# Optimization experiments

Hardware: AMD Instinct MI355X
Metric: run time of the kernel (lower is better)

## Reference

```python
import jax, jax.numpy as jnp
import numpy as np

B, S, D, VOCAB = 1024, 200, 128, 100000
MIN_LEN = 10


def setup_inputs() -> dict:
    key = jax.random.key(0)
    k1, k2, k3 = jax.random.split(key, 3)
    # variable per-row lengths; nonzero tokens contiguous at sequence start (right-padded)
    lengths = jax.random.randint(k1, (B,), MIN_LEN, S + 1)
    vals = jax.random.randint(k2, (B, S), 1, VOCAB)
    pos = jnp.arange(S)
    seqs = jnp.where(pos[None, :] < lengths[:, None], vals, 0)
    seq_embeddings = jax.random.normal(k3, (B, S, D), dtype=jnp.float32)
    return {"seqs": seqs, "seq_embeddings": seq_embeddings}


def _fft_prob(seqs):
    # Per-row: binary indicator of (token == last real token) over the L real
    # tokens, length-L DFT magnitude, zero last bin, normalize, roll by 1,
    # zero-pad to S. Variable-length FFT is written as an explicit DFT so the
    # whole batch is one dense einsum (same math as torch.fft.fft on length L).
    b, s = seqs.shape
    pos = jnp.arange(s)
    L = jnp.sum(seqs != 0, axis=1)                       # [B] real lengths
    last = seqs[jnp.arange(b), L - 1]                    # last real POI per row
    valid = pos[None, :] < L[:, None]                    # [B,S]
    binary = ((seqs == last[:, None]) & valid).astype(jnp.float32)  # [B,S]
    # DFT_k = sum_{n<L} binary_n * exp(-2*pi*i*k*n/L); binary is 0 for n>=L
    kn = (pos[:, None] * pos[None, :]).astype(jnp.float32)           # [S,S]
    theta = (-2.0 * jnp.pi) * kn[None, :, :] / L[:, None, None].astype(jnp.float32)  # [B,S,S]
    re = jnp.einsum('bkn,bn->bk', jnp.cos(theta), binary)
    im = jnp.einsum('bkn,bn->bk', jnp.sin(theta), binary)
    mag = jnp.sqrt(re * re + im * im)                    # [B,S] |FFT|
    # fft_prob[-1] = 0 (bin L-1) and bins k>=L are padding -> keep k < L-1
    keep = pos[None, :] < (L - 1)[:, None]
    mag = jnp.where(keep, mag, 0.0)
    prob = mag / jnp.sum(mag, axis=1, keepdims=True)
    # torch.roll(shifts=1) over the length-L vector: rolled[0]=prob[L-1]=0,
    # rolled[k]=prob[k-1]; since prob[k]=0 for k>=L-1 this equals a global
    # right-shift-by-one with zero fill, then implicit zero pad to S.
    rolled = jnp.pad(prob[:, :-1], ((0, 0), (1, 0)))
    return rolled                                         # [B,S]


def reference(seqs, seq_embeddings):
    prob = _fft_prob(seqs)                                # [B,S]
    return jnp.einsum('bs,bsd->bd', prob, seq_embeddings)  # [B,D]
```

## Files before the change

### kernel.cpp

```cpp
#include <hip/hip_runtime.h>
#include <math.h>

#define BATCH 1024
#define SEQ   200
#define DIM   128

__global__ __launch_bounds__(256) void dft_layer_kernel(
    const int* __restrict__ seqs,
    const float* __restrict__ emb,
    float* __restrict__ out)
{
    const int b   = blockIdx.x;
    const int tid = threadIdx.x;

    __shared__ int   s_seq[SEQ];
    __shared__ float s_mag[SEQ];
    __shared__ int   s_match[SEQ];
    __shared__ int   s_cnt[2];
    __shared__ float s_sum;
    __shared__ float s_part[8][DIM];

    if (tid < 2)  s_cnt[tid] = 0;
    if (tid == 0) s_sum = 0.0f;
    if (tid < SEQ) s_seq[tid] = seqs[b * SEQ + tid];
    __syncthreads();

    bool nz = (tid < SEQ) && (s_seq[tid] != 0);
    unsigned long long bal = __ballot(nz);
    if ((tid & 63) == 0) atomicAdd(&s_cnt[0], __popcll(bal));
    __syncthreads();

    const int L    = s_cnt[0];
    const int last = s_seq[L - 1];

    if (tid < L && s_seq[tid] == last) {
        int idx = atomicAdd(&s_cnt[1], 1);
        s_match[idx] = tid;
    }
    __syncthreads();
    const int   M  = s_cnt[1];
    const float Lf = (float)L;

    float mag = 0.0f;
    if (tid < SEQ) {
        if (tid < L - 1) {
            float re = 0.0f, im = 0.0f;
            const float kf = (float)tid;
            for (int m = 0; m < M; ++m) {
                float kn    = kf * (float)s_match[m];
                float theta = (-6.2831855f * kn) / Lf;
                float sv, cv;
                sincosf(theta, &sv, &cv);
                re += cv;
                im += sv;
            }
            mag = sqrtf(re * re + im * im);
        }
        s_mag[tid] = mag;
    }
    float v = mag;
    #pragma unroll
    for (int o = 32; o > 0; o >>= 1) v += __shfl_down(v, o, 64);
    if ((tid & 63) == 0) atomicAdd(&s_sum, v);
    __syncthreads();
    const float invSum = 1.0f / s_sum;

    const int c4 = tid & 31;
    const int g  = tid >> 5;
    const float4* ebase = (const float4*)(emb + (size_t)b * SEQ * DIM);
    float4 acc = make_float4(0.f, 0.f, 0.f, 0.f);
    for (int s = 1 + g; s < L; s += 8) {
        float  w = s_mag[s - 1];
        float4 e = ebase[s * 32 + c4];
        acc.x += w * e.x; acc.y += w * e.y; acc.z += w * e.z; acc.w += w * e.w;
    }
    {
        float* p = &s_part[g][c4 << 2];
        p[0] = acc.x; p[1] = acc.y; p[2] = acc.z; p[3] = acc.w;
    }
    __syncthreads();
    if (tid < DIM) {
        float r = 0.0f;
        #pragma unroll
        for (int gg = 0; gg < 8; ++gg) r += s_part[gg][tid];
        out[(size_t)b * DIM + tid] = r * invSum;
    }
}

extern "C" void kernel_launch(void* const* d_in, const int* in_sizes, int n_in,
                              void* d_out, int out_size, void* d_ws, size_t ws_size,
                              hipStream_t stream) {
    const int*   seqs = (const int*)d_in[0];
    const float* emb  = (const float*)d_in[1];
    float*       out  = (float*)d_out;
    dft_layer_kernel<<<BATCH, 256, 0, stream>>>(seqs, emb, out);
}
```

Baseline: 17.26 us.

## Add single-match fast path, fast trig with range reduction, wider blocks with dual accumulators

Adds a fast path for rows where the last token occurs only once: every DFT magnitude is then 1, so the DFT and the reduction are skipped and the weights become a uniform 1/(L-1). The general path now reduces the phase to [0,1) in revolutions and uses __sinf/__cosf in place of sincosf. The block grows to 512 threads with 16 row groups, and each thread keeps two accumulators to expose more memory-level parallelism in the weighted embedding sum. The fast intrinsics may lose some accuracy, and the larger block raises the cost of each barrier.

Measured after the change: 15.94 us. 7.6% less time.

```diff
diff --git a/kernel.cpp b/kernel.cpp
--- a/kernel.cpp
+++ b/kernel.cpp
@@ -4,8 +4,9 @@
 #define BATCH 1024
 #define SEQ   200
 #define DIM   128
+#define NT    512
 
-__global__ __launch_bounds__(256) void dft_layer_kernel(
+__global__ __launch_bounds__(NT, 8) void dft_layer_kernel(
     const int* __restrict__ seqs,
     const float* __restrict__ emb,
     float* __restrict__ out)
@@ -18,71 +19,98 @@
     __shared__ int   s_match[SEQ];
     __shared__ int   s_cnt[2];
     __shared__ float s_sum;
-    __shared__ float s_part[8][DIM];
+    __shared__ float s_part[16][DIM];
 
     if (tid < 2)  s_cnt[tid] = 0;
     if (tid == 0) s_sum = 0.0f;
-    if (tid < SEQ) s_seq[tid] = seqs[b * SEQ + tid];
+    int tok = 0;
+    if (tid < SEQ) { tok = seqs[b * SEQ + tid]; s_seq[tid] = tok; }
     __syncthreads();
 
-    bool nz = (tid < SEQ) && (s_seq[tid] != 0);
-    unsigned long long bal = __ballot(nz);
+    unsigned long long bal = __ballot((tid < SEQ) && (tok != 0));
     if ((tid & 63) == 0) atomicAdd(&s_cnt[0], __popcll(bal));
     __syncthreads();
-
     const int L    = s_cnt[0];
     const int last = s_seq[L - 1];
 
-    if (tid < L && s_seq[tid] == last) {
+    if ((tid < L) && (tok == last)) {
         int idx = atomicAdd(&s_cnt[1], 1);
         s_match[idx] = tid;
     }
     __syncthreads();
-    const int   M  = s_cnt[1];
-    const float Lf = (float)L;
+    const int M = s_cnt[1];
 
-    float mag = 0.0f;
-    if (tid < SEQ) {
+    float invSum;
+    if (M == 1) {
+        invSum = 1.0f / (float)(L - 1);
+    } else {
+        const float Lf = (float)L;
+        float mag = 0.0f;
         if (tid < L - 1) {
             float re = 0.0f, im = 0.0f;
             const float kf = (float)tid;
             for (int m = 0; m < M; ++m) {
-                float kn    = kf * (float)s_match[m];
-                float theta = (-6.2831855f * kn) / Lf;
-                float sv, cv;
-                sincosf(theta, &sv, &cv);
-                re += cv;
-                im += sv;
+                float rev = kf * (float)s_match[m] / Lf;
+                rev -= floorf(rev);
+                float th = 6.2831855f * rev;
+                re += __cosf(th);
+                im += __sinf(th);
             }
             mag = sqrtf(re * re + im * im);
         }
-        s_mag[tid] = mag;
+        if (tid < SEQ) s_mag[tid] = mag;
+        float v = mag;
+        #pragma unroll
+        for (int o = 32; o > 0; o >>= 1) v += __shfl_down(v, o, 64);
+        if ((tid & 63) == 0) atomicAdd(&s_sum, v);
+        __syncthreads();
+        invSum = 1.0f / s_sum;
     }
-    float v = mag;
-    #pragma unroll
-    for (int o = 32; o > 0; o >>= 1) v += __shfl_down(v, o, 64);
-    if ((tid & 63) == 0) atomicAdd(&s_sum, v);
-    __syncthreads();
-    const float invSum = 1.0f / s_sum;
 
     const int c4 = tid & 31;
     const int g  = tid >> 5;
     const float4* ebase = (const float4*)(emb + (size_t)b * SEQ * DIM);
-    float4 acc = make_float4(0.f, 0.f, 0.f, 0.f);
-    for (int s = 1 + g; s < L; s += 8) {
-        float  w = s_mag[s - 1];
-        float4 e = ebase[s * 32 + c4];
-        acc.x += w * e.x; acc.y += w * e.y; acc.z += w * e.z; acc.w += w * e.w;
+    float4 a0 = make_float4(0.f, 0.f, 0.f, 0.f);
+    float4 a1 = make_float4(0.f, 0.f, 0.f, 0.f);
+
+    if (M == 1) {
+        int s = 1 + g;
+        for (; s + 16 < L; s += 32) {
+            float4 e0 = ebase[s * 32 + c4];
+            float4 e1 = ebase[(s + 16) * 32 + c4];
+            a0.x += e0.x; a0.y += e0.y; a0.z += e0.z; a0.w += e0.w;
+            a1.x += e1.x; a1.y += e1.y; a1.z += e1.z; a1.w += e1.w;
+        }
+        if (s < L) {
+            float4 e0 = ebase[s * 32 + c4];
+            a0.x += e0.x; a0.y += e0.y; a0.z += e0.z; a0.w += e0.w;
+        }
+    } else {
+        int s = 1 + g;
+        for (; s + 16 < L; s += 32) {
+            float w0 = s_mag[s - 1];
+            float w1 = s_mag[s + 15];
+            float4 e0 = ebase[s * 32 + c4];
+            float4 e1 = ebase[(s + 16) * 32 + c4];
+            a0.x += w0 * e0.x; a0.y += w0 * e0.y; a0.z += w0 * e0.z; a0.w += w0 * e0.w;
+            a1.x += w1 * e1.x; a1.y += w1 * e1.y; a1.z += w1 * e1.z; a1.w += w1 * e1.w;
+        }
+        if (s < L) {
+            float w0 = s_mag[s - 1];
+            float4 e0 = ebase[s * 32 + c4];
+            a0.x += w0 * e0.x; a0.y += w0 * e0.y; a0.z += w0 * e0.z; a0.w += w0 * e0.w;
+        }
     }
+    a0.x += a1.x; a0.y += a1.y; a0.z += a1.z; a0.w += a1.w;
     {
         float* p = &s_part[g][c4 << 2];
-        p[0] = acc.x; p[1] = acc.y; p[2] = acc.z; p[3] = acc.w;
+        p[0] = a0.x; p[1] = a0.y; p[2] = a0.z; p[3] = a0.w;
     }
     __syncthreads();
     if (tid < DIM) {
         float r = 0.0f;
         #pragma unroll
-        for (int gg = 0; gg < 8; ++gg) r += s_part[gg][tid];
+        for (int gg = 0; gg < 16; ++gg) r += s_part[gg][tid];
         out[(size_t)b * DIM + tid] = r * invSum;
     }
 }
@@ -93,5 +121,5 @@
     const int*   seqs = (const int*)d_in[0];
     const float* emb  = (const float*)d_in[1];
     float*       out  = (float*)d_out;
-    dft_layer_kernel<<<BATCH, 256, 0, stream>>>(seqs, emb, out);
+    dft_layer_kernel<<<BATCH, NT, 0, stream>>>(seqs, emb, out);
 }
```
